# Optimization experiments

Measured on AMD Instinct MI355X. Metric: run time of the kernel, lower is better.

The kernel has to match this reference:

```python
import jax, jax.numpy as jnp
import numpy as np

B = 2097152   # rays
TS = 2048     # texture_size
C = 8         # num_channels
H1, H2 = 16, 16


def setup_inputs() -> dict:
    key = jax.random.key(0)
    ks = jax.random.split(key, 10)
    uv = jax.random.uniform(ks[0], (B, 2), jnp.float32) * 2.0 - 1.0  # [-1,1]
    vd = jax.random.normal(ks[1], (B, 3), jnp.float32)
    viewdirs = vd / jnp.linalg.norm(vd, axis=-1, keepdims=True)
    texture = jax.random.normal(ks[2], (1, C, TS, TS), jnp.float32) * 0.1
    in_dim = C + 3
    w1 = jax.random.normal(ks[3], (H1, in_dim), jnp.float32) * (1.0 / np.sqrt(in_dim))
    b1 = jnp.zeros((H1,), jnp.float32)
    w2 = jax.random.normal(ks[4], (H2, H1), jnp.float32) * (1.0 / np.sqrt(H1))
    b2 = jnp.zeros((H2,), jnp.float32)
    w3 = jax.random.normal(ks[5], (3, H2), jnp.float32) * (1.0 / np.sqrt(H2))
    b3 = jnp.zeros((3,), jnp.float32)
    return dict(uv=uv, viewdirs=viewdirs, texture=texture,
                w1=w1, b1=b1, w2=w2, b2=b2, w3=w3, b3=b3)


def _bilinear_sample(texture, uv):
    # texture: [1,C,H,W]; uv: [B,2] in [-1,1]; align_corners=True, border padding
    tex = jnp.transpose(texture[0], (1, 2, 0))  # [H,W,C]
    Ht, Wt = tex.shape[0], tex.shape[1]
    x = jnp.clip((uv[:, 0] + 1.0) * 0.5 * (Wt - 1), 0.0, Wt - 1)
    y = jnp.clip((uv[:, 1] + 1.0) * 0.5 * (Ht - 1), 0.0, Ht - 1)
    x0 = jnp.floor(x)
    y0 = jnp.floor(y)
    wx = (x - x0)[:, None]
    wy = (y - y0)[:, None]
    x0i = x0.astype(jnp.int32)
    y0i = y0.astype(jnp.int32)
    x1i = jnp.minimum(x0i + 1, Wt - 1)
    y1i = jnp.minimum(y0i + 1, Ht - 1)
    f00 = tex[y0i, x0i]  # [B,C]
    f01 = tex[y0i, x1i]
    f10 = tex[y1i, x0i]
    f11 = tex[y1i, x1i]
    return (f00 * (1 - wx) * (1 - wy) + f01 * wx * (1 - wy)
            + f10 * (1 - wx) * wy + f11 * wx * wy)


def reference(uv, viewdirs, texture, w1, b1, w2, b2, w3, b3):
    feat = _bilinear_sample(texture, uv)            # [B,C]
    x = jnp.concatenate([feat, viewdirs], axis=-1)  # [B,C+3]
    h = jax.nn.relu(x @ w1.T + b1)
    h = jax.nn.relu(h @ w2.T + b2)
    rgb = jax.nn.sigmoid(h @ w3.T + b3)             # [B,3]
    return rgb
```

## Files before the change

### kernel.cpp

```cpp
#include <hip/hip_runtime.h>
#include <hip/hip_bf16.h>

#define TSZ 2048
#define NCH 8
#define NPIX (TSZ * TSZ)

__device__ __forceinline__ unsigned pack_bf16_rne(float a, float b) {
    unsigned ua = __float_as_uint(a);
    unsigned ub = __float_as_uint(b);
    ua += 0x7fffu + ((ua >> 16) & 1u);
    ub += 0x7fffu + ((ub >> 16) & 1u);
    return (ua >> 16) | (ub & 0xffff0000u);
}
__device__ __forceinline__ float blo(unsigned u) { return __uint_as_float(u << 16); }
__device__ __forceinline__ float bhi(unsigned u) { return __uint_as_float(u & 0xffff0000u); }

__global__ __launch_bounds__(256) void transpose_pack_kernel(
    const float* __restrict__ tex, uint4* __restrict__ txp)
{
    const int p = blockIdx.x * 256 + threadIdx.x;
    float v[NCH];
#pragma unroll
    for (int c = 0; c < NCH; ++c)
        v[c] = tex[(size_t)c * NPIX + p];
    uint4 q;
    q.x = pack_bf16_rne(v[0], v[1]);
    q.y = pack_bf16_rne(v[2], v[3]);
    q.z = pack_bf16_rne(v[4], v[5]);
    q.w = pack_bf16_rne(v[6], v[7]);
    txp[p] = q;
}

__global__ __launch_bounds__(256) void gather_mlp_kernel(
    const float* __restrict__ uv,
    const float* __restrict__ vd,
    const uint4* __restrict__ txp,
    const float* __restrict__ w1, const float* __restrict__ b1,
    const float* __restrict__ w2, const float* __restrict__ b2,
    const float* __restrict__ w3, const float* __restrict__ b3,
    float* __restrict__ out, int B)
{
    __shared__ float sw1[16 * 11];
    __shared__ float sb1[16];
    __shared__ float sw2[16 * 16];
    __shared__ float sb2[16];
    __shared__ float sw3[3 * 16];
    __shared__ float sb3[3];

    const int t = threadIdx.x;
    for (int i = t; i < 16 * 11; i += 256) sw1[i] = w1[i];
    for (int i = t; i < 16 * 16; i += 256) sw2[i] = w2[i];
    for (int i = t; i < 3 * 16;  i += 256) sw3[i] = w3[i];
    if (t < 16) { sb1[t] = b1[t]; sb2[t] = b2[t]; }
    if (t < 3)  { sb3[t] = b3[t]; }
    __syncthreads();

    const int idx = blockIdx.x * 256 + t;
    if (idx >= B) return;

    const float2 uv2 = reinterpret_cast<const float2*>(uv)[idx];
    const float fx = fminf(fmaxf((uv2.x + 1.0f) * 0.5f * (float)(TSZ - 1), 0.0f), (float)(TSZ - 1));
    const float fy = fminf(fmaxf((uv2.y + 1.0f) * 0.5f * (float)(TSZ - 1), 0.0f), (float)(TSZ - 1));
    const float x0f = floorf(fx);
    const float y0f = floorf(fy);
    const float wx = fx - x0f;
    const float wy = fy - y0f;
    const int x0 = (int)x0f;
    const int y0 = (int)y0f;
    const int x1 = min(x0 + 1, TSZ - 1);
    const int y1 = min(y0 + 1, TSZ - 1);

    const float w00 = (1.0f - wx) * (1.0f - wy);
    const float w01 = wx * (1.0f - wy);
    const float w10 = (1.0f - wx) * wy;
    const float w11 = wx * wy;

    const uint4 q00 = txp[(size_t)y0 * TSZ + x0];
    const uint4 q01 = txp[(size_t)y0 * TSZ + x1];
    const uint4 q10 = txp[(size_t)y1 * TSZ + x0];
    const uint4 q11 = txp[(size_t)y1 * TSZ + x1];

    float xin[11];
    xin[0] = blo(q00.x) * w00 + blo(q01.x) * w01 + blo(q10.x) * w10 + blo(q11.x) * w11;
    xin[1] = bhi(q00.x) * w00 + bhi(q01.x) * w01 + bhi(q10.x) * w10 + bhi(q11.x) * w11;
    xin[2] = blo(q00.y) * w00 + blo(q01.y) * w01 + blo(q10.y) * w10 + blo(q11.y) * w11;
    xin[3] = bhi(q00.y) * w00 + bhi(q01.y) * w01 + bhi(q10.y) * w10 + bhi(q11.y) * w11;
    xin[4] = blo(q00.z) * w00 + blo(q01.z) * w01 + blo(q10.z) * w10 + blo(q11.z) * w11;
    xin[5] = bhi(q00.z) * w00 + bhi(q01.z) * w01 + bhi(q10.z) * w10 + bhi(q11.z) * w11;
    xin[6] = blo(q00.w) * w00 + blo(q01.w) * w01 + blo(q10.w) * w10 + blo(q11.w) * w11;
    xin[7] = bhi(q00.w) * w00 + bhi(q01.w) * w01 + bhi(q10.w) * w10 + bhi(q11.w) * w11;
    xin[8]  = vd[3 * (size_t)idx + 0];
    xin[9]  = vd[3 * (size_t)idx + 1];
    xin[10] = vd[3 * (size_t)idx + 2];

    float h1[16];
#pragma unroll
    for (int j = 0; j < 16; ++j) {
        float a = sb1[j];
#pragma unroll
        for (int i = 0; i < 11; ++i) a += xin[i] * sw1[j * 11 + i];
        h1[j] = fmaxf(a, 0.0f);
    }

    float h2[16];
#pragma unroll
    for (int j = 0; j < 16; ++j) {
        float a = sb2[j];
#pragma unroll
        for (int i = 0; i < 16; ++i) a += h1[i] * sw2[j * 16 + i];
        h2[j] = fmaxf(a, 0.0f);
    }

    float rgb[3];
#pragma unroll
    for (int k = 0; k < 3; ++k) {
        float a = sb3[k];
#pragma unroll
        for (int i = 0; i < 16; ++i) a += h2[i] * sw3[k * 16 + i];
        rgb[k] = 1.0f / (1.0f + __expf(-a));
    }

    out[3 * (size_t)idx + 0] = rgb[0];
    out[3 * (size_t)idx + 1] = rgb[1];
    out[3 * (size_t)idx + 2] = rgb[2];
}

__global__ __launch_bounds__(256) void hybrid_texmlp_kernel(
    const float* __restrict__ uv,
    const float* __restrict__ vd,
    const float* __restrict__ tex,
    const float* __restrict__ w1, const float* __restrict__ b1,
    const float* __restrict__ w2, const float* __restrict__ b2,
    const float* __restrict__ w3, const float* __restrict__ b3,
    float* __restrict__ out, int B)
{
    __shared__ float sw1[16 * 11];
    __shared__ float sb1[16];
    __shared__ float sw2[16 * 16];
    __shared__ float sb2[16];
    __shared__ float sw3[3 * 16];
    __shared__ float sb3[3];

    const int t = threadIdx.x;
    for (int i = t; i < 16 * 11; i += 256) sw1[i] = w1[i];
    for (int i = t; i < 16 * 16; i += 256) sw2[i] = w2[i];
    for (int i = t; i < 3 * 16;  i += 256) sw3[i] = w3[i];
    if (t < 16) { sb1[t] = b1[t]; sb2[t] = b2[t]; }
    if (t < 3)  { sb3[t] = b3[t]; }
    __syncthreads();

    const int idx = blockIdx.x * 256 + t;
    if (idx >= B) return;

    const float2 uv2 = reinterpret_cast<const float2*>(uv)[idx];
    const float fx = fminf(fmaxf((uv2.x + 1.0f) * 0.5f * (float)(TSZ - 1), 0.0f), (float)(TSZ - 1));
    const float fy = fminf(fmaxf((uv2.y + 1.0f) * 0.5f * (float)(TSZ - 1), 0.0f), (float)(TSZ - 1));
    const float x0f = floorf(fx);
    const float y0f = floorf(fy);
    const float wx = fx - x0f;
    const float wy = fy - y0f;
    const int x0 = (int)x0f;
    const int y0 = (int)y0f;
    const int x1 = min(x0 + 1, TSZ - 1);
    const int y1 = min(y0 + 1, TSZ - 1);

    const float w00 = (1.0f - wx) * (1.0f - wy);
    const float w01 = wx * (1.0f - wy);
    const float w10 = (1.0f - wx) * wy;
    const float w11 = wx * wy;

    const size_t o00 = (size_t)y0 * TSZ + x0;
    const size_t o01 = (size_t)y0 * TSZ + x1;
    const size_t o10 = (size_t)y1 * TSZ + x0;
    const size_t o11 = (size_t)y1 * TSZ + x1;

    float xin[11];
#pragma unroll
    for (int c = 0; c < NCH; ++c) {
        const float* __restrict__ p = tex + (size_t)c * NPIX;
        xin[c] = p[o00] * w00 + p[o01] * w01 + p[o10] * w10 + p[o11] * w11;
    }
    xin[8]  = vd[3 * (size_t)idx + 0];
    xin[9]  = vd[3 * (size_t)idx + 1];
    xin[10] = vd[3 * (size_t)idx + 2];

    float h1[16];
#pragma unroll
    for (int j = 0; j < 16; ++j) {
        float a = sb1[j];
#pragma unroll
        for (int i = 0; i < 11; ++i) a += xin[i] * sw1[j * 11 + i];
        h1[j] = fmaxf(a, 0.0f);
    }
    float h2[16];
#pragma unroll
    for (int j = 0; j < 16; ++j) {
        float a = sb2[j];
#pragma unroll
        for (int i = 0; i < 16; ++i) a += h1[i] * sw2[j * 16 + i];
        h2[j] = fmaxf(a, 0.0f);
    }
    float rgb[3];
#pragma unroll
    for (int k = 0; k < 3; ++k) {
        float a = sb3[k];
#pragma unroll
        for (int i = 0; i < 16; ++i) a += h2[i] * sw3[k * 16 + i];
        rgb[k] = 1.0f / (1.0f + __expf(-a));
    }

    out[3 * (size_t)idx + 0] = rgb[0];
    out[3 * (size_t)idx + 1] = rgb[1];
    out[3 * (size_t)idx + 2] = rgb[2];
}

extern "C" void kernel_launch(void* const* d_in, const int* in_sizes, int n_in,
                              void* d_out, int out_size, void* d_ws, size_t ws_size,
                              hipStream_t stream) {
    const float* uv  = (const float*)d_in[0];
    const float* vd  = (const float*)d_in[1];
    const float* tex = (const float*)d_in[2];
    const float* w1  = (const float*)d_in[3];
    const float* b1  = (const float*)d_in[4];
    const float* w2  = (const float*)d_in[5];
    const float* b2  = (const float*)d_in[6];
    const float* w3  = (const float*)d_in[7];
    const float* b3  = (const float*)d_in[8];
    float* out = (float*)d_out;

    const int B = in_sizes[0] / 2;
    const int block = 256;
    const int grid = (B + block - 1) / block;

    const size_t need = (size_t)NPIX * 16;
    if (ws_size >= need) {
        uint4* txp = (uint4*)d_ws;
        transpose_pack_kernel<<<NPIX / block, block, 0, stream>>>(tex, txp);
        gather_mlp_kernel<<<grid, block, 0, stream>>>(
            uv, vd, txp, w1, b1, w2, b2, w3, b3, out, B);
    } else {
        hybrid_texmlp_kernel<<<grid, block, 0, stream>>>(
            uv, vd, tex, w1, b1, w2, b2, w3, b3, out, B);
    }
}
```

Measured before the change: 325.5 us.

## Pack bilinear quads contiguously so each ray fetches one 64-byte block

```diff
diff --git a/kernel.cpp b/kernel.cpp
--- a/kernel.cpp
+++ b/kernel.cpp
@@ -15,26 +15,43 @@
 __device__ __forceinline__ float blo(unsigned u) { return __uint_as_float(u << 16); }
 __device__ __forceinline__ float bhi(unsigned u) { return __uint_as_float(u & 0xffff0000u); }
 
-__global__ __launch_bounds__(256) void transpose_pack_kernel(
-    const float* __restrict__ tex, uint4* __restrict__ txp)
-{
-    const int p = blockIdx.x * 256 + threadIdx.x;
-    float v[NCH];
-#pragma unroll
-    for (int c = 0; c < NCH; ++c)
-        v[c] = tex[(size_t)c * NPIX + p];
-    uint4 q;
-    q.x = pack_bf16_rne(v[0], v[1]);
-    q.y = pack_bf16_rne(v[2], v[3]);
-    q.z = pack_bf16_rne(v[4], v[5]);
-    q.w = pack_bf16_rne(v[6], v[7]);
-    txp[p] = q;
-}
-
-__global__ __launch_bounds__(256) void gather_mlp_kernel(
+__global__ __launch_bounds__(256) void quad_pack_kernel(
+    const float* __restrict__ tex, uint4* __restrict__ txq)
+{
+    const int q = blockIdx.x * 256 + threadIdx.x;
+    const int y = q >> 11;
+    const int x = q & (TSZ - 1);
+    const int x1 = min(x + 1, TSZ - 1);
+    const int y1 = min(y + 1, TSZ - 1);
+    const size_t o00 = (size_t)y  * TSZ + x;
+    const size_t o01 = (size_t)y  * TSZ + x1;
+    const size_t o10 = (size_t)y1 * TSZ + x;
+    const size_t o11 = (size_t)y1 * TSZ + x1;
+
+    float a[NCH], b[NCH], c[NCH], d[NCH];
+#pragma unroll
+    for (int ch = 0; ch < NCH; ++ch) {
+        const float* __restrict__ p = tex + (size_t)ch * NPIX;
+        a[ch] = p[o00];
+        b[ch] = p[o01];
+        c[ch] = p[o10];
+        d[ch] = p[o11];
+    }
+    uint4* dst = txq + (size_t)q * 4;
+    dst[0] = make_uint4(pack_bf16_rne(a[0], a[1]), pack_bf16_rne(a[2], a[3]),
+                        pack_bf16_rne(a[4], a[5]), pack_bf16_rne(a[6], a[7]));
+    dst[1] = make_uint4(pack_bf16_rne(b[0], b[1]), pack_bf16_rne(b[2], b[3]),
+                        pack_bf16_rne(b[4], b[5]), pack_bf16_rne(b[6], b[7]));
+    dst[2] = make_uint4(pack_bf16_rne(c[0], c[1]), pack_bf16_rne(c[2], c[3]),
+                        pack_bf16_rne(c[4], c[5]), pack_bf16_rne(c[6], c[7]));
+    dst[3] = make_uint4(pack_bf16_rne(d[0], d[1]), pack_bf16_rne(d[2], d[3]),
+                        pack_bf16_rne(d[4], d[5]), pack_bf16_rne(d[6], d[7]));
+}
+
+__global__ __launch_bounds__(256) void gather_quad_kernel(
     const float* __restrict__ uv,
     const float* __restrict__ vd,
-    const uint4* __restrict__ txp,
+    const uint4* __restrict__ txq,
     const float* __restrict__ w1, const float* __restrict__ b1,
     const float* __restrict__ w2, const float* __restrict__ b2,
     const float* __restrict__ w3, const float* __restrict__ b3,
@@ -67,18 +84,17 @@
     const float wy = fy - y0f;
     const int x0 = (int)x0f;
     const int y0 = (int)y0f;
-    const int x1 = min(x0 + 1, TSZ - 1);
-    const int y1 = min(y0 + 1, TSZ - 1);
 
     const float w00 = (1.0f - wx) * (1.0f - wy);
     const float w01 = wx * (1.0f - wy);
     const float w10 = (1.0f - wx) * wy;
     const float w11 = wx * wy;
 
-    const uint4 q00 = txp[(size_t)y0 * TSZ + x0];
-    const uint4 q01 = txp[(size_t)y0 * TSZ + x1];
-    const uint4 q10 = txp[(size_t)y1 * TSZ + x0];
-    const uint4 q11 = txp[(size_t)y1 * TSZ + x1];
+    const uint4* qb = txq + ((size_t)y0 * TSZ + x0) * 4;
+    const uint4 q00 = qb[0];
+    const uint4 q01 = qb[1];
+    const uint4 q10 = qb[2];
+    const uint4 q11 = qb[3];
 
     float xin[11];
     xin[0] = blo(q00.x) * w00 + blo(q01.x) * w01 + blo(q10.x) * w10 + blo(q11.x) * w11;
@@ -101,7 +117,6 @@
         for (int i = 0; i < 11; ++i) a += xin[i] * sw1[j * 11 + i];
         h1[j] = fmaxf(a, 0.0f);
     }
-
     float h2[16];
 #pragma unroll
     for (int j = 0; j < 16; ++j) {
@@ -110,7 +125,118 @@
         for (int i = 0; i < 16; ++i) a += h1[i] * sw2[j * 16 + i];
         h2[j] = fmaxf(a, 0.0f);
     }
-
+    float rgb[3];
+#pragma unroll
+    for (int k = 0; k < 3; ++k) {
+        float a = sb3[k];
+#pragma unroll
+        for (int i = 0; i < 16; ++i) a += h2[i] * sw3[k * 16 + i];
+        rgb[k] = 1.0f / (1.0f + __expf(-a));
+    }
+
+    out[3 * (size_t)idx + 0] = rgb[0];
+    out[3 * (size_t)idx + 1] = rgb[1];
+    out[3 * (size_t)idx + 2] = rgb[2];
+}
+
+__global__ __launch_bounds__(256) void transpose_pack4_kernel(
+    const float* __restrict__ tex, uint4* __restrict__ txp)
+{
+    const int p4 = (blockIdx.x * 256 + threadIdx.x) * 4;
+    float4 v[NCH];
+#pragma unroll
+    for (int c = 0; c < NCH; ++c)
+        v[c] = *reinterpret_cast<const float4*>(tex + (size_t)c * NPIX + p4);
+    const float* vf = reinterpret_cast<const float*>(v);
+#pragma unroll
+    for (int i = 0; i < 4; ++i) {
+        uint4 qq;
+        qq.x = pack_bf16_rne(vf[0 * 4 + i], vf[1 * 4 + i]);
+        qq.y = pack_bf16_rne(vf[2 * 4 + i], vf[3 * 4 + i]);
+        qq.z = pack_bf16_rne(vf[4 * 4 + i], vf[5 * 4 + i]);
+        qq.w = pack_bf16_rne(vf[6 * 4 + i], vf[7 * 4 + i]);
+        txp[p4 + i] = qq;
+    }
+}
+
+__global__ __launch_bounds__(256) void gather_mlp_kernel(
+    const float* __restrict__ uv,
+    const float* __restrict__ vd,
+    const uint4* __restrict__ txp,
+    const float* __restrict__ w1, const float* __restrict__ b1,
+    const float* __restrict__ w2, const float* __restrict__ b2,
+    const float* __restrict__ w3, const float* __restrict__ b3,
+    float* __restrict__ out, int B)
+{
+    __shared__ float sw1[16 * 11];
+    __shared__ float sb1[16];
+    __shared__ float sw2[16 * 16];
+    __shared__ float sb2[16];
+    __shared__ float sw3[3 * 16];
+    __shared__ float sb3[3];
+
+    const int t = threadIdx.x;
+    for (int i = t; i < 16 * 11; i += 256) sw1[i] = w1[i];
+    for (int i = t; i < 16 * 16; i += 256) sw2[i] = w2[i];
+    for (int i = t; i < 3 * 16;  i += 256) sw3[i] = w3[i];
+    if (t < 16) { sb1[t] = b1[t]; sb2[t] = b2[t]; }
+    if (t < 3)  { sb3[t] = b3[t]; }
+    __syncthreads();
+
+    const int idx = blockIdx.x * 256 + t;
+    if (idx >= B) return;
+
+    const float2 uv2 = reinterpret_cast<const float2*>(uv)[idx];
+    const float fx = fminf(fmaxf((uv2.x + 1.0f) * 0.5f * (float)(TSZ - 1), 0.0f), (float)(TSZ - 1));
+    const float fy = fminf(fmaxf((uv2.y + 1.0f) * 0.5f * (float)(TSZ - 1), 0.0f), (float)(TSZ - 1));
+    const float x0f = floorf(fx);
+    const float y0f = floorf(fy);
+    const float wx = fx - x0f;
+    const float wy = fy - y0f;
+    const int x0 = (int)x0f;
+    const int y0 = (int)y0f;
+    const int x1 = min(x0 + 1, TSZ - 1);
+    const int y1 = min(y0 + 1, TSZ - 1);
+
+    const float w00 = (1.0f - wx) * (1.0f - wy);
+    const float w01 = wx * (1.0f - wy);
+    const float w10 = (1.0f - wx) * wy;
+    const float w11 = wx * wy;
+
+    const uint4 q00 = txp[(size_t)y0 * TSZ + x0];
+    const uint4 q01 = txp[(size_t)y0 * TSZ + x1];
+    const uint4 q10 = txp[(size_t)y1 * TSZ + x0];
+    const uint4 q11 = txp[(size_t)y1 * TSZ + x1];
+
+    float xin[11];
+    xin[0] = blo(q00.x) * w00 + blo(q01.x) * w01 + blo(q10.x) * w10 + blo(q11.x) * w11;
+    xin[1] = bhi(q00.x) * w00 + bhi(q01.x) * w01 + bhi(q10.x) * w10 + bhi(q11.x) * w11;
+    xin[2] = blo(q00.y) * w00 + blo(q01.y) * w01 + blo(q10.y) * w10 + blo(q11.y) * w11;
+    xin[3] = bhi(q00.y) * w00 + bhi(q01.y) * w01 + bhi(q10.y) * w10 + bhi(q11.y) * w11;
+    xin[4] = blo(q00.z) * w00 + blo(q01.z) * w01 + blo(q10.z) * w10 + blo(q11.z) * w11;
+    xin[5] = bhi(q00.z) * w00 + bhi(q01.z) * w01 + bhi(q10.z) * w10 + bhi(q11.z) * w11;
+    xin[6] = blo(q00.w) * w00 + blo(q01.w) * w01 + blo(q10.w) * w10 + blo(q11.w) * w11;
+    xin[7] = bhi(q00.w) * w00 + bhi(q01.w) * w01 + bhi(q10.w) * w10 + bhi(q11.w) * w11;
+    xin[8]  = vd[3 * (size_t)idx + 0];
+    xin[9]  = vd[3 * (size_t)idx + 1];
+    xin[10] = vd[3 * (size_t)idx + 2];
+
+    float h1[16];
+#pragma unroll
+    for (int j = 0; j < 16; ++j) {
+        float a = sb1[j];
+#pragma unroll
+        for (int i = 0; i < 11; ++i) a += xin[i] * sw1[j * 11 + i];
+        h1[j] = fmaxf(a, 0.0f);
+    }
+    float h2[16];
+#pragma unroll
+    for (int j = 0; j < 16; ++j) {
+        float a = sb2[j];
+#pragma unroll
+        for (int i = 0; i < 16; ++i) a += h1[i] * sw2[j * 16 + i];
+        h2[j] = fmaxf(a, 0.0f);
+    }
     float rgb[3];
 #pragma unroll
     for (int k = 0; k < 3; ++k) {
@@ -232,10 +358,17 @@
     const int block = 256;
     const int grid = (B + block - 1) / block;
 
-    const size_t need = (size_t)NPIX * 16;
-    if (ws_size >= need) {
+    const size_t need_quad = (size_t)NPIX * 64;
+    const size_t need_flat = (size_t)NPIX * 16;
+
+    if (ws_size >= need_quad) {
+        uint4* txq = (uint4*)d_ws;
+        quad_pack_kernel<<<NPIX / block, block, 0, stream>>>(tex, txq);
+        gather_quad_kernel<<<grid, block, 0, stream>>>(
+            uv, vd, txq, w1, b1, w2, b2, w3, b3, out, B);
+    } else if (ws_size >= need_flat) {
         uint4* txp = (uint4*)d_ws;
-        transpose_pack_kernel<<<NPIX / block, block, 0, stream>>>(tex, txp);
+        transpose_pack4_kernel<<<NPIX / (block * 4), block, 0, stream>>>(tex, txp);
         gather_mlp_kernel<<<grid, block, 0, stream>>>(
             uv, vd, txp, w1, b1, w2, b2, w3, b3, out, B);
     } else {
```

Result: slower. 405.4 us (+24.5%).
